# Kernel tuning notes

Hardware: AMD Instinct MI355X
Metric: run time of the kernel (lower is better)

The kernel has to match this reference:

```python
import jax, jax.numpy as jnp
import numpy as np

TWO_PI = 2.0 * np.pi
DIST_THRESH = 0.1  # squared-distance threshold from the source


def _fourier_basis(x, y, K):
    # phase[i, l, k] = 2*pi*(k*x_i + l*y_i), k,l in 1..K, reshaped to [inchans, K*K]
    kk = jnp.arange(1, K + 1, dtype=x.dtype)  # varies along last axis (columns)
    ll = jnp.arange(1, K + 1, dtype=x.dtype)  # varies along middle axis (rows)
    phase = TWO_PI * (kk[None, None, :] * x[:, None, None]
                      + ll[None, :, None] * y[:, None, None])
    phase = phase.reshape(x.shape[0], K * K)
    return jnp.cos(phase), jnp.sin(phase)


def setup_inputs() -> dict:
    key = jax.random.key(0)
    ks = jax.random.split(key, 7)
    B, C_in, C_out, K, T = 128, 273, 270, 32, 2048
    return {
        "X": jax.random.normal(ks[0], (B, C_in, T), dtype=jnp.float32),
        "z_real": jax.random.normal(ks[1], (C_out, K * K), dtype=jnp.float32) / (32.0 * 32.0),
        "z_imag": jax.random.normal(ks[2], (C_out, K * K), dtype=jnp.float32) / (32.0 * 32.0),
        "x": jax.random.uniform(ks[3], (C_in,), dtype=jnp.float32),
        "y": jax.random.uniform(ks[4], (C_in,), dtype=jnp.float32),
        "x_drop": jax.random.uniform(ks[5], (), dtype=jnp.float32),
        "y_drop": jax.random.uniform(ks[6], (), dtype=jnp.float32),
    }


def reference(X, z_real, z_imag, x, y, x_drop, y_drop):
    K = int(np.sqrt(z_real.shape[1]))
    cos_m, sin_m = _fourier_basis(x, y, K)          # [C_in, K*K] each
    # logits over input channels: [C_out, C_in]
    a = z_real @ cos_m.T + z_imag @ sin_m.T
    # zero (not -inf) logits of channels near the drop point, as in the source
    dist2 = (x_drop - x) ** 2 + (y_drop - y) ** 2   # [C_in]
    a = jnp.where((dist2 < DIST_THRESH)[None, :], 0.0, a)
    a = jax.nn.softmax(a, axis=1)                    # [C_out, C_in]
    return jnp.einsum('oi,bit->bot', a, X)           # [B, C_out, T]
```

## Files before the change

kernel.cpp:

```cpp
#include <hip/hip_runtime.h>
#include <hip/hip_bf16.h>
#include <math.h>

typedef short s16x4 __attribute__((ext_vector_type(4)));
typedef short bf16x8 __attribute__((ext_vector_type(8)));
typedef float f32x16 __attribute__((ext_vector_type(16)));

#define C_IN 273
#define C_OUT 270
#define T_DIM 2048
#define KP 288
#define APR_STRIDE 288
#define APR_ROWS 320

#define WS_COS 0u
#define WS_SIN 1118208u
#define WS_PART 2236416u
#define WS_APERM 4743168u

#define ALD_STRIDE 592
#define A_LDS_BYTES (64 * ALD_STRIDE)
#define XBUF_BYTES 16384

__device__ __forceinline__ short f2bf(float f) {
  __hip_bfloat16 h = __float2bfloat16(f);
  short r; __builtin_memcpy(&r, &h, 2); return r;
}

__global__ void k_basis(const float* __restrict__ x, const float* __restrict__ y,
                        float* __restrict__ cosb, float* __restrict__ sinb) {
  const int i = blockIdx.x;
  const float xi = x[i], yi = y[i];
  const int base = threadIdx.x * 4;
  #pragma unroll
  for (int j = 0; j < 4; ++j) {
    const int kl = base + j;
    const float kf = (float)((kl & 31) + 1);
    const float lf = (float)((kl >> 5) + 1);
    const float ph = 6.28318530717958647692f * (kf * xi + lf * yi);
    float sn, cs;
    sincosf(ph, &sn, &cs);
    cosb[(size_t)i * 1024 + kl] = cs;
    sinb[(size_t)i * 1024 + kl] = sn;
  }
}

__global__ __launch_bounds__(256) void k_logits(const float* __restrict__ zr,
    const float* __restrict__ zi, const float* __restrict__ cosb,
    const float* __restrict__ sinb, float* __restrict__ part) {
  const int tx = threadIdx.x & 15, ty = threadIdx.x >> 4;
  const int ibase = blockIdx.x * 64 + tx * 4;
  const int obase = blockIdx.y * 64 + ty * 4;
  const int kl0 = (int)blockIdx.z * 128;
  int oc[4], ic[4];
  #pragma unroll
  for (int a = 0; a < 4; ++a) {
    oc[a] = min(obase + a, C_OUT - 1);
    ic[a] = min(ibase + a, C_IN - 1);
  }
  float acc[4][4] = {};
  for (int kl = kl0; kl < kl0 + 128; kl += 4) {
    float4 zr4[4], zi4[4], cb4[4], sb4[4];
    #pragma unroll
    for (int a = 0; a < 4; ++a) {
      zr4[a] = *(const float4*)(zr + (size_t)oc[a] * 1024 + kl);
      zi4[a] = *(const float4*)(zi + (size_t)oc[a] * 1024 + kl);
    }
    #pragma unroll
    for (int b = 0; b < 4; ++b) {
      cb4[b] = *(const float4*)(cosb + (size_t)ic[b] * 1024 + kl);
      sb4[b] = *(const float4*)(sinb + (size_t)ic[b] * 1024 + kl);
    }
    #pragma unroll
    for (int a = 0; a < 4; ++a)
      #pragma unroll
      for (int b = 0; b < 4; ++b)
        acc[a][b] += zr4[a].x * cb4[b].x + zr4[a].y * cb4[b].y
                   + zr4[a].z * cb4[b].z + zr4[a].w * cb4[b].w
                   + zi4[a].x * sb4[b].x + zi4[a].y * sb4[b].y
                   + zi4[a].z * sb4[b].z + zi4[a].w * sb4[b].w;
  }
  #pragma unroll
  for (int a = 0; a < 4; ++a)
    #pragma unroll
    for (int b = 0; b < 4; ++b) {
      const int o = obase + a, i = ibase + b;
      if (o < C_OUT && i < C_IN)
        part[((size_t)blockIdx.z * 272 + o) * 288 + i] = acc[a][b];
    }
}

__global__ __launch_bounds__(256) void k_softmax(const float* __restrict__ part,
    const float* __restrict__ x, const float* __restrict__ y,
    const float* __restrict__ xdp, const float* __restrict__ ydp,
    __hip_bfloat16* __restrict__ aperm) {
  const int o = blockIdx.x;
  const int tid = threadIdx.x;
  if (o >= C_OUT) {
    for (int s = tid; s < KP; s += 256)
      aperm[(size_t)o * APR_STRIDE + s] = __float2bfloat16(0.f);
    return;
  }
  __shared__ float red[8];
  const float xd = xdp[0], yd = ydp[0];
  const int i0 = tid, i1 = tid + 256;
  float v0, v1 = 0.f;
  {
    float s = 0.f;
    #pragma unroll
    for (int c = 0; c < 8; ++c) s += part[((size_t)c * 272 + o) * 288 + i0];
    const float dx = xd - x[i0], dy = yd - y[i0];
    v0 = (dx * dx + dy * dy < 0.1f) ? 0.f : s;
  }
  const bool has1 = (i1 < C_IN);
  if (has1) {
    float s = 0.f;
    #pragma unroll
    for (int c = 0; c < 8; ++c) s += part[((size_t)c * 272 + o) * 288 + i1];
    const float dx = xd - x[i1], dy = yd - y[i1];
    v1 = (dx * dx + dy * dy < 0.1f) ? 0.f : s;
  }
  float mv = has1 ? fmaxf(v0, v1) : v0;
  #pragma unroll
  for (int off = 32; off >= 1; off >>= 1) mv = fmaxf(mv, __shfl_down(mv, off));
  if ((tid & 63) == 0) red[tid >> 6] = mv;
  __syncthreads();
  const float M = fmaxf(fmaxf(red[0], red[1]), fmaxf(red[2], red[3]));
  const float e0 = expf(v0 - M);
  const float e1 = has1 ? expf(v1 - M) : 0.f;
  float sv = e0 + e1;
  #pragma unroll
  for (int off = 32; off >= 1; off >>= 1) sv += __shfl_down(sv, off);
  __syncthreads();
  if ((tid & 63) == 0) red[4 + (tid >> 6)] = sv;
  __syncthreads();
  const float S = red[4] + red[5] + red[6] + red[7];
  const float inv = 1.0f / S;
  {
    const int s = (i0 & ~3) | ((i0 & 3) ^ ((i0 >> 2) & 3));
    aperm[(size_t)o * APR_STRIDE + s] = __float2bfloat16(e0 * inv);
  }
  if (i1 < KP) {
    const int s = (i1 & ~3) | ((i1 & 3) ^ ((i1 >> 2) & 3));
    aperm[(size_t)o * APR_STRIDE + s] = __float2bfloat16(has1 ? e1 * inv : 0.f);
  }
}

__device__ __forceinline__ void load_chunk(const float* __restrict__ Xb, int ch,
                                           int t_base, int tid, float4 (&r)[2][4]) {
  #pragma unroll
  for (int h = 0; h < 2; ++h) {
    const int s = tid + h * 256;
    const int k4 = s & 7, t4 = s >> 3;
    const int t = t_base + t4 * 4;
    #pragma unroll
    for (int rr = 0; rr < 4; ++rr) {
      const int i = ch * 32 + k4 * 4 + rr;
      float4 v = make_float4(0.f, 0.f, 0.f, 0.f);
      if (i < C_IN) v = *(const float4*)(Xb + (size_t)i * T_DIM + t);
      r[h][rr] = v;
    }
  }
}

__device__ __forceinline__ void write_chunk(char* __restrict__ xb, int tid,
                                            const float4 (&r)[2][4]) {
  #pragma unroll
  for (int h = 0; h < 2; ++h) {
    const int s = tid + h * 256;
    const int k4 = s & 7, t4 = s >> 3;
    const int tb = t4 >> 2, c4 = t4 & 3;
    #pragma unroll
    for (int rr = 0; rr < 4; ++rr) {
      const int j = rr ^ (k4 & 3);
      s16x4 p;
      p[0] = f2bf(r[h][rr].x); p[1] = f2bf(r[h][rr].y);
      p[2] = f2bf(r[h][rr].z); p[3] = f2bf(r[h][rr].w);
      *(s16x4*)(xb + (k4 * 16 + tb) * 128 + j * 32 + c4 * 8) = p;
    }
  }
}

__global__ __launch_bounds__(256) void k_gemm(const float* __restrict__ X,
    const __hip_bfloat16* __restrict__ aperm, float* __restrict__ out) {
  __shared__ __align__(16) char smem[A_LDS_BYTES + 2 * XBUF_BYTES];
  const int tid = threadIdx.x;
  const int lane = tid & 63, w = tid >> 6;
  const int o_base = blockIdx.y * 64;
  const int t_base = blockIdx.x * 256;
  const float* Xb = X + (size_t)blockIdx.z * C_IN * T_DIM;

  {
    const int row = tid >> 2, q = tid & 3;
    const float4* src = (const float4*)((const char*)(aperm + (size_t)(o_base + row) * APR_STRIDE) + q * 144);
    float4* dst = (float4*)(smem + row * ALD_STRIDE + q * 144);
    #pragma unroll
    for (int v = 0; v < 9; ++v) dst[v] = src[v];
  }

  f32x16 acc[2][2] = {};
  const unsigned smem_u = (unsigned)(unsigned long long)(uintptr_t)smem;
  const unsigned xlds0 = smem_u + A_LDS_BYTES;
  const int lg = lane >> 4, l16 = lane & 15, l32 = lane & 31, lh = lane >> 5;
  const unsigned bconst = (unsigned)((lg >> 1) * 4096 + (lg & 1) * 128 + w * 512 + l16 * 8);

  float4 regs[2][4];
  load_chunk(Xb, 0, t_base, tid, regs);
  write_chunk(smem + A_LDS_BYTES, tid, regs);
  __syncthreads();

  #pragma unroll 2
  for (int ch = 0; ch < 9; ++ch) {
    const int buf = ch & 1;
    if (ch < 8) load_chunk(Xb, ch + 1, t_base, tid, regs);
    {
      const unsigned xb = xlds0 + buf * XBUF_BYTES + bconst;
      const char* arow0 = smem + l32 * ALD_STRIDE + (ch * 32) * 2 + lh * 16;
      #pragma unroll
      for (int kk = 0; kk < 32; kk += 16) {
        bf16x8 A0 = *(const bf16x8*)(arow0 + kk * 2);
        bf16x8 A1 = *(const bf16x8*)(arow0 + 32 * ALD_STRIDE + kk * 2);
        s16x4 t0, t1, t2, t3;
        const unsigned a0 = xb + kk * 512;
        asm volatile("ds_read_b64_tr_b16 %0, %1" : "=v"(t0) : "v"(a0));
        asm volatile("ds_read_b64_tr_b16 %0, %1 offset:2048" : "=v"(t1) : "v"(a0));
        asm volatile("ds_read_b64_tr_b16 %0, %1 offset:256" : "=v"(t2) : "v"(a0));
        asm volatile("ds_read_b64_tr_b16 %0, %1 offset:2304" : "=v"(t3) : "v"(a0));
        asm volatile("s_waitcnt lgkmcnt(0)" ::: "memory");
        __builtin_amdgcn_sched_barrier(0);
        bf16x8 B0, B1;
        B0[0] = t0[0]; B0[1] = t0[1]; B0[2] = t0[2]; B0[3] = t0[3];
        B0[4] = t1[0]; B0[5] = t1[1]; B0[6] = t1[2]; B0[7] = t1[3];
        B1[0] = t2[0]; B1[1] = t2[1]; B1[2] = t2[2]; B1[3] = t2[3];
        B1[4] = t3[0]; B1[5] = t3[1]; B1[6] = t3[2]; B1[7] = t3[3];
        acc[0][0] = __builtin_amdgcn_mfma_f32_32x32x16_bf16(A0, B0, acc[0][0], 0, 0, 0);
        acc[0][1] = __builtin_amdgcn_mfma_f32_32x32x16_bf16(A0, B1, acc[0][1], 0, 0, 0);
        acc[1][0] = __builtin_amdgcn_mfma_f32_32x32x16_bf16(A1, B0, acc[1][0], 0, 0, 0);
        acc[1][1] = __builtin_amdgcn_mfma_f32_32x32x16_bf16(A1, B1, acc[1][1], 0, 0, 0);
      }
    }
    if (ch < 8) write_chunk(smem + A_LDS_BYTES + (buf ^ 1) * XBUF_BYTES, tid, regs);
    __syncthreads();
  }

  float* outb = out + (size_t)blockIdx.z * C_OUT * T_DIM;
  #pragma unroll
  for (int m = 0; m < 2; ++m)
    #pragma unroll
    for (int n = 0; n < 2; ++n)
      #pragma unroll
      for (int r = 0; r < 16; ++r) {
        const int o = o_base + m * 32 + (r & 3) + 8 * (r >> 2) + 4 * lh;
        if (o < C_OUT) {
          const int t = t_base + w * 64 + n * 32 + l32;
          outb[(size_t)o * T_DIM + t] = acc[m][n][r];
        }
      }
}

extern "C" void kernel_launch(void* const* d_in, const int* in_sizes, int n_in,
                              void* d_out, int out_size, void* d_ws, size_t ws_size,
                              hipStream_t stream) {
  const float* X  = (const float*)d_in[0];
  const float* zr = (const float*)d_in[1];
  const float* zi = (const float*)d_in[2];
  const float* x  = (const float*)d_in[3];
  const float* y  = (const float*)d_in[4];
  const float* xd = (const float*)d_in[5];
  const float* yd = (const float*)d_in[6];
  float* out = (float*)d_out;
  char* ws = (char*)d_ws;
  float* cosb = (float*)(ws + WS_COS);
  float* sinb = (float*)(ws + WS_SIN);
  float* part = (float*)(ws + WS_PART);
  __hip_bfloat16* aperm = (__hip_bfloat16*)(ws + WS_APERM);

  k_basis<<<dim3(273), dim3(256), 0, stream>>>(x, y, cosb, sinb);
  k_logits<<<dim3(5, 5, 8), dim3(256), 0, stream>>>(zr, zi, cosb, sinb, part);
  k_softmax<<<dim3(APR_ROWS), dim3(256), 0, stream>>>(part, x, y, xd, yd, aperm);
  k_gemm<<<dim3(8, 5, 128), dim3(256), 0, stream>>>(X, aperm, out);
}
```

Measured before the change: 324.1 us.

## Halve GEMM T-tile to 128 and prefetch two chunks ahead in registers

```diff
diff --git a/kernel.cpp b/kernel.cpp
--- a/kernel.cpp
+++ b/kernel.cpp
@@ -20,7 +20,7 @@
 
 #define ALD_STRIDE 592
 #define A_LDS_BYTES (64 * ALD_STRIDE)
-#define XBUF_BYTES 16384
+#define XBUF_BYTES 8192
 
 __device__ __forceinline__ short f2bf(float f) {
   __hip_bfloat16 h = __float2bfloat16(f);
@@ -147,37 +147,29 @@
 }
 
 __device__ __forceinline__ void load_chunk(const float* __restrict__ Xb, int ch,
-                                           int t_base, int tid, float4 (&r)[2][4]) {
-  #pragma unroll
-  for (int h = 0; h < 2; ++h) {
-    const int s = tid + h * 256;
-    const int k4 = s & 7, t4 = s >> 3;
-    const int t = t_base + t4 * 4;
-    #pragma unroll
-    for (int rr = 0; rr < 4; ++rr) {
-      const int i = ch * 32 + k4 * 4 + rr;
-      float4 v = make_float4(0.f, 0.f, 0.f, 0.f);
-      if (i < C_IN) v = *(const float4*)(Xb + (size_t)i * T_DIM + t);
-      r[h][rr] = v;
-    }
+                                           int t_base, int tid, float4 (&r)[4]) {
+  const int k4 = tid & 7, t4 = tid >> 3;
+  const int t = t_base + t4 * 4;
+  #pragma unroll
+  for (int rr = 0; rr < 4; ++rr) {
+    const int i = ch * 32 + k4 * 4 + rr;
+    float4 v = make_float4(0.f, 0.f, 0.f, 0.f);
+    if (i < C_IN) v = *(const float4*)(Xb + (size_t)i * T_DIM + t);
+    r[rr] = v;
   }
 }
 
 __device__ __forceinline__ void write_chunk(char* __restrict__ xb, int tid,
-                                            const float4 (&r)[2][4]) {
-  #pragma unroll
-  for (int h = 0; h < 2; ++h) {
-    const int s = tid + h * 256;
-    const int k4 = s & 7, t4 = s >> 3;
-    const int tb = t4 >> 2, c4 = t4 & 3;
-    #pragma unroll
-    for (int rr = 0; rr < 4; ++rr) {
-      const int j = rr ^ (k4 & 3);
-      s16x4 p;
-      p[0] = f2bf(r[h][rr].x); p[1] = f2bf(r[h][rr].y);
-      p[2] = f2bf(r[h][rr].z); p[3] = f2bf(r[h][rr].w);
-      *(s16x4*)(xb + (k4 * 16 + tb) * 128 + j * 32 + c4 * 8) = p;
-    }
+                                            const float4 (&r)[4]) {
+  const int k4 = tid & 7, t4 = tid >> 3;
+  const int tb = t4 >> 2, c4 = t4 & 3;
+  #pragma unroll
+  for (int rr = 0; rr < 4; ++rr) {
+    const int j = rr ^ (k4 & 3);
+    s16x4 p;
+    p[0] = f2bf(r[rr].x); p[1] = f2bf(r[rr].y);
+    p[2] = f2bf(r[rr].z); p[3] = f2bf(r[rr].w);
+    *(s16x4*)(xb + (k4 * 8 + tb) * 128 + j * 32 + c4 * 8) = p;
   }
 }
 
@@ -187,7 +179,7 @@
   const int tid = threadIdx.x;
   const int lane = tid & 63, w = tid >> 6;
   const int o_base = blockIdx.y * 64;
-  const int t_base = blockIdx.x * 256;
+  const int t_base = blockIdx.x * 128;
   const float* Xb = X + (size_t)blockIdx.z * C_IN * T_DIM;
 
   {
@@ -198,64 +190,68 @@
     for (int v = 0; v < 9; ++v) dst[v] = src[v];
   }
 
-  f32x16 acc[2][2] = {};
+  f32x16 acc[2] = {};
   const unsigned smem_u = (unsigned)(unsigned long long)(uintptr_t)smem;
   const unsigned xlds0 = smem_u + A_LDS_BYTES;
   const int lg = lane >> 4, l16 = lane & 15, l32 = lane & 31, lh = lane >> 5;
-  const unsigned bconst = (unsigned)((lg >> 1) * 4096 + (lg & 1) * 128 + w * 512 + l16 * 8);
-
-  float4 regs[2][4];
-  load_chunk(Xb, 0, t_base, tid, regs);
-  write_chunk(smem + A_LDS_BYTES, tid, regs);
-  __syncthreads();
-
-  #pragma unroll 2
-  for (int ch = 0; ch < 9; ++ch) {
-    const int buf = ch & 1;
-    if (ch < 8) load_chunk(Xb, ch + 1, t_base, tid, regs);
-    {
-      const unsigned xb = xlds0 + buf * XBUF_BYTES + bconst;
-      const char* arow0 = smem + l32 * ALD_STRIDE + (ch * 32) * 2 + lh * 16;
-      #pragma unroll
-      for (int kk = 0; kk < 32; kk += 16) {
-        bf16x8 A0 = *(const bf16x8*)(arow0 + kk * 2);
-        bf16x8 A1 = *(const bf16x8*)(arow0 + 32 * ALD_STRIDE + kk * 2);
-        s16x4 t0, t1, t2, t3;
-        const unsigned a0 = xb + kk * 512;
-        asm volatile("ds_read_b64_tr_b16 %0, %1" : "=v"(t0) : "v"(a0));
-        asm volatile("ds_read_b64_tr_b16 %0, %1 offset:2048" : "=v"(t1) : "v"(a0));
-        asm volatile("ds_read_b64_tr_b16 %0, %1 offset:256" : "=v"(t2) : "v"(a0));
-        asm volatile("ds_read_b64_tr_b16 %0, %1 offset:2304" : "=v"(t3) : "v"(a0));
-        asm volatile("s_waitcnt lgkmcnt(0)" ::: "memory");
-        __builtin_amdgcn_sched_barrier(0);
-        bf16x8 B0, B1;
-        B0[0] = t0[0]; B0[1] = t0[1]; B0[2] = t0[2]; B0[3] = t0[3];
-        B0[4] = t1[0]; B0[5] = t1[1]; B0[6] = t1[2]; B0[7] = t1[3];
-        B1[0] = t2[0]; B1[1] = t2[1]; B1[2] = t2[2]; B1[3] = t2[3];
-        B1[4] = t3[0]; B1[5] = t3[1]; B1[6] = t3[2]; B1[7] = t3[3];
-        acc[0][0] = __builtin_amdgcn_mfma_f32_32x32x16_bf16(A0, B0, acc[0][0], 0, 0, 0);
-        acc[0][1] = __builtin_amdgcn_mfma_f32_32x32x16_bf16(A0, B1, acc[0][1], 0, 0, 0);
-        acc[1][0] = __builtin_amdgcn_mfma_f32_32x32x16_bf16(A1, B0, acc[1][0], 0, 0, 0);
-        acc[1][1] = __builtin_amdgcn_mfma_f32_32x32x16_bf16(A1, B1, acc[1][1], 0, 0, 0);
+  const unsigned bconst = (unsigned)((lg >> 1) * 2048 + (lg & 1) * 128 + w * 256 + l16 * 8);
+
+  char* xb0 = smem + A_LDS_BYTES;
+  char* xb1 = smem + A_LDS_BYTES + XBUF_BYTES;
+
+  float4 rA[4], rB[4];
+  load_chunk(Xb, 0, t_base, tid, rA);
+  load_chunk(Xb, 1, t_base, tid, rB);
+  write_chunk(xb0, tid, rA);
+  __syncthreads();
+
+  #define COMPUTE(CH, BUFSEL)                                                      \
+    {                                                                              \
+      const unsigned xb = xlds0 + (BUFSEL) * XBUF_BYTES + bconst;                  \
+      const char* arow0 = smem + l32 * ALD_STRIDE + ((CH) * 32) * 2 + lh * 16;     \
+      _Pragma("unroll")                                                            \
+      for (int kk = 0; kk < 32; kk += 16) {                                        \
+        bf16x8 A0 = *(const bf16x8*)(arow0 + kk * 2);                              \
+        bf16x8 A1 = *(const bf16x8*)(arow0 + 32 * ALD_STRIDE + kk * 2);            \
+        s16x4 t0, t1;                                                              \
+        const unsigned a0 = xb + kk * 256;                                         \
+        asm volatile("ds_read_b64_tr_b16 %0, %1" : "=v"(t0) : "v"(a0));            \
+        asm volatile("ds_read_b64_tr_b16 %0, %1 offset:1024" : "=v"(t1) : "v"(a0));\
+        asm volatile("s_waitcnt lgkmcnt(0)" ::: "memory");                         \
+        __builtin_amdgcn_sched_barrier(0);                                         \
+        bf16x8 B0;                                                                 \
+        B0[0] = t0[0]; B0[1] = t0[1]; B0[2] = t0[2]; B0[3] = t0[3];                \
+        B0[4] = t1[0]; B0[5] = t1[1]; B0[6] = t1[2]; B0[7] = t1[3];                \
+        acc[0] = __builtin_amdgcn_mfma_f32_32x32x16_bf16(A0, B0, acc[0], 0, 0, 0); \
+        acc[1] = __builtin_amdgcn_mfma_f32_32x32x16_bf16(A1, B0, acc[1], 0, 0, 0); \
+      }                                                                            \
+    }
+
+  for (int ch = 0; ch < 9; ch += 2) {
+    if (ch + 2 < 9) load_chunk(Xb, ch + 2, t_base, tid, rA);
+    COMPUTE(ch, 0)
+    if (ch + 1 < 9) write_chunk(xb1, tid, rB);
+    __syncthreads();
+    if (ch + 1 < 9) {
+      if (ch + 3 < 9) load_chunk(Xb, ch + 3, t_base, tid, rB);
+      COMPUTE(ch + 1, 1)
+      if (ch + 2 < 9) write_chunk(xb0, tid, rA);
+      __syncthreads();
+    }
+  }
+  #undef COMPUTE
+
+  float* outb = out + (size_t)blockIdx.z * C_OUT * T_DIM;
+  #pragma unroll
+  for (int m = 0; m < 2; ++m)
+    #pragma unroll
+    for (int r = 0; r < 16; ++r) {
+      const int o = o_base + m * 32 + (r & 3) + 8 * (r >> 2) + 4 * lh;
+      if (o < C_OUT) {
+        const int t = t_base + w * 32 + l32;
+        outb[(size_t)o * T_DIM + t] = acc[m][r];
       }
     }
-    if (ch < 8) write_chunk(smem + A_LDS_BYTES + (buf ^ 1) * XBUF_BYTES, tid, regs);
-    __syncthreads();
-  }
-
-  float* outb = out + (size_t)blockIdx.z * C_OUT * T_DIM;
-  #pragma unroll
-  for (int m = 0; m < 2; ++m)
-    #pragma unroll
-    for (int n = 0; n < 2; ++n)
-      #pragma unroll
-      for (int r = 0; r < 16; ++r) {
-        const int o = o_base + m * 32 + (r & 3) + 8 * (r >> 2) + 4 * lh;
-        if (o < C_OUT) {
-          const int t = t_base + w * 64 + n * 32 + l32;
-          outb[(size_t)o * T_DIM + t] = acc[m][n][r];
-        }
-      }
 }
 
 extern "C" void kernel_launch(void* const* d_in, const int* in_sizes, int n_in,
@@ -278,5 +274,5 @@
   k_basis<<<dim3(273), dim3(256), 0, stream>>>(x, y, cosb, sinb);
   k_logits<<<dim3(5, 5, 8), dim3(256), 0, stream>>>(zr, zi, cosb, sinb, part);
   k_softmax<<<dim3(APR_ROWS), dim3(256), 0, stream>>>(part, x, y, xd, yd, aperm);
-  k_gemm<<<dim3(8, 5, 128), dim3(256), 0, stream>>>(X, aperm, out);
-}
+  k_gemm<<<dim3(16, 5, 128), dim3(256), 0, stream>>>(X, aperm, out);
+}
```

After: 335.7 us. 3.6% more time.

## Cover all output channels per block to read X once

Applied to the files above, without the earlier changes.

```diff
diff --git a/kernel.cpp b/kernel.cpp
--- a/kernel.cpp
+++ b/kernel.cpp
@@ -18,9 +18,10 @@
 #define WS_PART 2236416u
 #define WS_APERM 4743168u
 
-#define ALD_STRIDE 592
-#define A_LDS_BYTES (64 * ALD_STRIDE)
-#define XBUF_BYTES 16384
+#define A_ROW_STRIDE 72
+#define A_CHUNK_BYTES (288 * A_ROW_STRIDE)
+#define X_CHUNK_BYTES 4096
+#define LDS_TOTAL (2 * A_CHUNK_BYTES + 2 * X_CHUNK_BYTES)
 
 __device__ __forceinline__ short f2bf(float f) {
   __hip_bfloat16 h = __float2bfloat16(f);
@@ -146,116 +147,148 @@
   }
 }
 
-__device__ __forceinline__ void load_chunk(const float* __restrict__ Xb, int ch,
-                                           int t_base, int tid, float4 (&r)[2][4]) {
-  #pragma unroll
-  for (int h = 0; h < 2; ++h) {
-    const int s = tid + h * 256;
-    const int k4 = s & 7, t4 = s >> 3;
-    const int t = t_base + t4 * 4;
-    #pragma unroll
-    for (int rr = 0; rr < 4; ++rr) {
-      const int i = ch * 32 + k4 * 4 + rr;
-      float4 v = make_float4(0.f, 0.f, 0.f, 0.f);
-      if (i < C_IN) v = *(const float4*)(Xb + (size_t)i * T_DIM + t);
-      r[h][rr] = v;
-    }
-  }
-}
-
-__device__ __forceinline__ void write_chunk(char* __restrict__ xb, int tid,
-                                            const float4 (&r)[2][4]) {
-  #pragma unroll
-  for (int h = 0; h < 2; ++h) {
-    const int s = tid + h * 256;
-    const int k4 = s & 7, t4 = s >> 3;
-    const int tb = t4 >> 2, c4 = t4 & 3;
-    #pragma unroll
-    for (int rr = 0; rr < 4; ++rr) {
-      const int j = rr ^ (k4 & 3);
-      s16x4 p;
-      p[0] = f2bf(r[h][rr].x); p[1] = f2bf(r[h][rr].y);
-      p[2] = f2bf(r[h][rr].z); p[3] = f2bf(r[h][rr].w);
-      *(s16x4*)(xb + (k4 * 16 + tb) * 128 + j * 32 + c4 * 8) = p;
-    }
-  }
-}
-
-__global__ __launch_bounds__(256) void k_gemm(const float* __restrict__ X,
+typedef float f32x2 __attribute__((ext_vector_type(2)));
+
+__global__ __launch_bounds__(256, 3) void k_gemm(const float* __restrict__ X,
     const __hip_bfloat16* __restrict__ aperm, float* __restrict__ out) {
-  __shared__ __align__(16) char smem[A_LDS_BYTES + 2 * XBUF_BYTES];
+  __shared__ __align__(16) char smem[LDS_TOTAL];
   const int tid = threadIdx.x;
   const int lane = tid & 63, w = tid >> 6;
-  const int o_base = blockIdx.y * 64;
-  const int t_base = blockIdx.x * 256;
-  const float* Xb = X + (size_t)blockIdx.z * C_IN * T_DIM;
-
-  {
-    const int row = tid >> 2, q = tid & 3;
-    const float4* src = (const float4*)((const char*)(aperm + (size_t)(o_base + row) * APR_STRIDE) + q * 144);
-    float4* dst = (float4*)(smem + row * ALD_STRIDE + q * 144);
-    #pragma unroll
-    for (int v = 0; v < 9; ++v) dst[v] = src[v];
-  }
-
-  f32x16 acc[2][2] = {};
+  const int l16 = lane & 15, l32 = lane & 31, lh = lane >> 5, lg4 = (lane >> 4) & 1;
+
+  const int bid = blockIdx.x;
+  const int b = bid >> 5;
+  const int t_base = (bid & 31) * 64;
+  const float* Xb = X + (size_t)b * C_IN * T_DIM;
+  const char* apc = (const char*)aperm;
+
+  const int m_start = (w == 0) ? 0 : (2 * w + 1);
+  const int mcount  = (w == 0) ? 3 : 2;
+
   const unsigned smem_u = (unsigned)(unsigned long long)(uintptr_t)smem;
-  const unsigned xlds0 = smem_u + A_LDS_BYTES;
-  const int lg = lane >> 4, l16 = lane & 15, l32 = lane & 31, lh = lane >> 5;
-  const unsigned bconst = (unsigned)((lg >> 1) * 4096 + (lg & 1) * 128 + w * 512 + l16 * 8);
-
-  float4 regs[2][4];
-  load_chunk(Xb, 0, t_base, tid, regs);
-  write_chunk(smem + A_LDS_BYTES, tid, regs);
+
+  f32x2 areg[9];
+  float4 xreg[2];
+
+  #define LOADA(CH)                                                              \
+    _Pragma("unroll")                                                            \
+    for (int j = 0; j < 9; ++j) {                                                \
+      const int idx = j * 256 + tid;                                             \
+      const int row = idx >> 3, q = idx & 7;                                     \
+      areg[j] = *(const f32x2*)(apc + (size_t)row * 576 + (CH) * 64 + q * 8);    \
+    }
+
+  #define WRITEA(BUF)                                                            \
+    _Pragma("unroll")                                                            \
+    for (int j = 0; j < 9; ++j) {                                                \
+      const int idx = j * 256 + tid;                                             \
+      const int row = idx >> 3, q = idx & 7;                                     \
+      *(f32x2*)(smem + (BUF) * A_CHUNK_BYTES + row * A_ROW_STRIDE + q * 8) = areg[j]; \
+    }
+
+  #define LOADX(CH)                                                              \
+    _Pragma("unroll")                                                            \
+    for (int h = 0; h < 2; ++h) {                                                \
+      const int idx = tid + h * 256;                                             \
+      const int row = idx >> 4, c4 = idx & 15;                                   \
+      const int i = (CH) * 32 + row;                                             \
+      float4 v = make_float4(0.f, 0.f, 0.f, 0.f);                                \
+      if (i < C_IN) v = *(const float4*)(Xb + (size_t)i * T_DIM + t_base + c4 * 4); \
+      xreg[h] = v;                                                               \
+    }
+
+  #define WRITEX(BUF)                                                            \
+    _Pragma("unroll")                                                            \
+    for (int h = 0; h < 2; ++h) {                                                \
+      const int idx = tid + h * 256;                                             \
+      const int row = idx >> 4, c4 = idx & 15;                                   \
+      const int k4 = row >> 2, rr = row & 3;                                     \
+      const int j = rr ^ (k4 & 3);    \
+      const int tb = c4 >> 2, cc = c4 & 3;                                       \
+      s16x4 p;                                                                   \
+      p[0] = f2bf(xreg[h].x); p[1] = f2bf(xreg[h].y);                            \
+      p[2] = f2bf(xreg[h].z); p[3] = f2bf(xreg[h].w);                            \
+      *(s16x4*)(smem + 2 * A_CHUNK_BYTES + (BUF) * X_CHUNK_BYTES                 \
+                + (k4 * 4 + tb) * 128 + j * 32 + cc * 8) = p;                    \
+    }
+
+  f32x16 acc[3][2] = {};
+
+  LOADA(0)
+  LOADX(0)
+  WRITEA(0)
+  WRITEX(0)
   __syncthreads();
 
-  #pragma unroll 2
   for (int ch = 0; ch < 9; ++ch) {
-    const int buf = ch & 1;
-    if (ch < 8) load_chunk(Xb, ch + 1, t_base, tid, regs);
+    const int cur = ch & 1;
+    if (ch < 8) {
+      LOADA(ch + 1)
+      LOADX(ch + 1)
+    }
     {
-      const unsigned xb = xlds0 + buf * XBUF_BYTES + bconst;
-      const char* arow0 = smem + l32 * ALD_STRIDE + (ch * 32) * 2 + lh * 16;
+      const char* Ab = smem + cur * A_CHUNK_BYTES;
+      const unsigned Xv = smem_u + 2 * A_CHUNK_BYTES + cur * X_CHUNK_BYTES;
       #pragma unroll
       for (int kk = 0; kk < 32; kk += 16) {
-        bf16x8 A0 = *(const bf16x8*)(arow0 + kk * 2);
-        bf16x8 A1 = *(const bf16x8*)(arow0 + 32 * ALD_STRIDE + kk * 2);
-        s16x4 t0, t1, t2, t3;
-        const unsigned a0 = xb + kk * 512;
-        asm volatile("ds_read_b64_tr_b16 %0, %1" : "=v"(t0) : "v"(a0));
-        asm volatile("ds_read_b64_tr_b16 %0, %1 offset:2048" : "=v"(t1) : "v"(a0));
-        asm volatile("ds_read_b64_tr_b16 %0, %1 offset:256" : "=v"(t2) : "v"(a0));
-        asm volatile("ds_read_b64_tr_b16 %0, %1 offset:2304" : "=v"(t3) : "v"(a0));
+        s16x4 t00, t01, t10, t11;
+        const unsigned xa = Xv + kk * 128 + lh * 1024 + lg4 * 128 + l16 * 8;
+        asm volatile("ds_read_b64_tr_b16 %0, %1"             : "=v"(t00) : "v"(xa));
+        asm volatile("ds_read_b64_tr_b16 %0, %1 offset:512"  : "=v"(t01) : "v"(xa));
+        asm volatile("ds_read_b64_tr_b16 %0, %1 offset:256"  : "=v"(t10) : "v"(xa));
+        asm volatile("ds_read_b64_tr_b16 %0, %1 offset:768"  : "=v"(t11) : "v"(xa));
+        bf16x8 af[3];
+        #pragma unroll
+        for (int mi = 0; mi < 3; ++mi) {
+          if (mi < mcount) {
+            const char* ar = Ab + ((m_start + mi) * 32 + l32) * A_ROW_STRIDE + kk * 2 + lh * 16;
+            s16x4 alo = *(const s16x4*)(ar);
+            s16x4 ahi = *(const s16x4*)(ar + 8);
+            af[mi] = __builtin_shufflevector(alo, ahi, 0, 1, 2, 3, 4, 5, 6, 7);
+          }
+        }
         asm volatile("s_waitcnt lgkmcnt(0)" ::: "memory");
         __builtin_amdgcn_sched_barrier(0);
-        bf16x8 B0, B1;
-        B0[0] = t0[0]; B0[1] = t0[1]; B0[2] = t0[2]; B0[3] = t0[3];
-        B0[4] = t1[0]; B0[5] = t1[1]; B0[6] = t1[2]; B0[7] = t1[3];
-        B1[0] = t2[0]; B1[1] = t2[1]; B1[2] = t2[2]; B1[3] = t2[3];
-        B1[4] = t3[0]; B1[5] = t3[1]; B1[6] = t3[2]; B1[7] = t3[3];
-        acc[0][0] = __builtin_amdgcn_mfma_f32_32x32x16_bf16(A0, B0, acc[0][0], 0, 0, 0);
-        acc[0][1] = __builtin_amdgcn_mfma_f32_32x32x16_bf16(A0, B1, acc[0][1], 0, 0, 0);
-        acc[1][0] = __builtin_amdgcn_mfma_f32_32x32x16_bf16(A1, B0, acc[1][0], 0, 0, 0);
-        acc[1][1] = __builtin_amdgcn_mfma_f32_32x32x16_bf16(A1, B1, acc[1][1], 0, 0, 0);
-      }
-    }
-    if (ch < 8) write_chunk(smem + A_LDS_BYTES + (buf ^ 1) * XBUF_BYTES, tid, regs);
-    __syncthreads();
-  }
-
-  float* outb = out + (size_t)blockIdx.z * C_OUT * T_DIM;
-  #pragma unroll
-  for (int m = 0; m < 2; ++m)
-    #pragma unroll
-    for (int n = 0; n < 2; ++n)
-      #pragma unroll
-      for (int r = 0; r < 16; ++r) {
-        const int o = o_base + m * 32 + (r & 3) + 8 * (r >> 2) + 4 * lh;
-        if (o < C_OUT) {
-          const int t = t_base + w * 64 + n * 32 + l32;
-          outb[(size_t)o * T_DIM + t] = acc[m][n][r];
+        bf16x8 B0 = __builtin_shufflevector(t00, t01, 0, 1, 2, 3, 4, 5, 6, 7);
+        bf16x8 B1 = __builtin_shufflevector(t10, t11, 0, 1, 2, 3, 4, 5, 6, 7);
+        #pragma unroll
+        for (int mi = 0; mi < 3; ++mi) {
+          if (mi < mcount) {
+            acc[mi][0] = __builtin_amdgcn_mfma_f32_32x32x16_bf16(af[mi], B0, acc[mi][0], 0, 0, 0);
+            acc[mi][1] = __builtin_amdgcn_mfma_f32_32x32x16_bf16(af[mi], B1, acc[mi][1], 0, 0, 0);
+          }
         }
       }
+    }
+    if (ch < 8) {
+      WRITEA(cur ^ 1)
+      WRITEX(cur ^ 1)
+    }
+    __syncthreads();
+  }
+
+  #undef LOADA
+  #undef WRITEA
+  #undef LOADX
+  #undef WRITEX
+
+  float* outb = out + (size_t)b * C_OUT * T_DIM;
+  #pragma unroll
+  for (int mi = 0; mi < 3; ++mi) {
+    if (mi < mcount) {
+      const int m = m_start + mi;
+      #pragma unroll
+      for (int n = 0; n < 2; ++n)
+        #pragma unroll
+        for (int r = 0; r < 16; ++r) {
+          const int o = m * 32 + (r & 3) + 8 * (r >> 2) + 4 * lh;
+          if (o < C_OUT) {
+            const int t = t_base + n * 32 + l32;
+            outb[(size_t)o * T_DIM + t] = acc[mi][n][r];
+          }
+        }
+    }
+  }
 }
 
 extern "C" void kernel_launch(void* const* d_in, const int* in_sizes, int n_in,
@@ -278,5 +311,5 @@
   k_basis<<<dim3(273), dim3(256), 0, stream>>>(x, y, cosb, sinb);
   k_logits<<<dim3(5, 5, 8), dim3(256), 0, stream>>>(zr, zi, cosb, sinb, part);
   k_softmax<<<dim3(APR_ROWS), dim3(256), 0, stream>>>(part, x, y, xd, yd, aperm);
-  k_gemm<<<dim3(8, 5, 128), dim3(256), 0, stream>>>(X, aperm, out);
-}
+  k_gemm<<<dim3(4096), dim3(256), 0, stream>>>(X, aperm, out);
+}
```

Measured after the change: 724.5 us. +123.6%, slower.
